# Kernel optimization log

Measured on AMD Instinct MI355X. Metric: run time of the kernel, lower is better.

Reference implementation:

```python
import jax, jax.numpy as jnp
import numpy as np

N_EMBD = 512
N_HEAD = 8
HEAD_DIM = N_EMBD // N_HEAD


def setup_inputs() -> dict:
    key = jax.random.key(0)
    ks = jax.random.split(key, 10)
    B, Tx, Tc, C = 8, 1024, 2048, N_EMBD
    s = 1.0 / np.sqrt(C)
    return {
        "x": jax.random.normal(ks[0], (B, Tx, C), dtype=jnp.float32),
        "context": jax.random.normal(ks[1], (B, Tc, C), dtype=jnp.float32),
        "Wq": jax.random.normal(ks[2], (C, C), dtype=jnp.float32) * s,
        "bq": jnp.zeros((C,), dtype=jnp.float32),
        "Wk": jax.random.normal(ks[3], (C, C), dtype=jnp.float32) * s,
        "bk": jnp.zeros((C,), dtype=jnp.float32),
        "Wv": jax.random.normal(ks[4], (C, C), dtype=jnp.float32) * s,
        "bv": jnp.zeros((C,), dtype=jnp.float32),
        "Wo": jax.random.normal(ks[5], (C, C), dtype=jnp.float32) * s,
        "bo": jnp.zeros((C,), dtype=jnp.float32),
    }


def reference(x, context, Wq, bq, Wk, bk, Wv, bv, Wo, bo):
    B, Tx, C = x.shape
    Tc = context.shape[1]
    nh, hd = N_HEAD, C // N_HEAD
    # projections (torch Linear: y = x @ W.T + b)
    q = (x @ Wq.T + bq).reshape(B, Tx, nh, hd).transpose(0, 2, 1, 3)
    k = (context @ Wk.T + bk).reshape(B, Tc, nh, hd).transpose(0, 2, 1, 3)
    v = (context @ Wv.T + bv).reshape(B, Tc, nh, hd).transpose(0, 2, 1, 3)
    # attention scores (B, nh, Tx, Tc)
    att = jnp.einsum("bhqd,bhkd->bhqk", q, k) * (1.0 / np.sqrt(hd))
    att = jax.nn.softmax(att, axis=-1)
    y = jnp.einsum("bhqk,bhkd->bhqd", att, v)
    y = y.transpose(0, 2, 1, 3).reshape(B, Tx, C)
    att_mean = att.mean(axis=1)  # (B, Tx, Tc)
    y = y @ Wo.T + bo
    return (y, att_mean)
```

## Files before the change

### kernel.cpp

```cpp
#include <hip/hip_runtime.h>

#define DEVI __device__ __forceinline__

typedef short bf16x8 __attribute__((ext_vector_type(8)));
typedef short bf16x4 __attribute__((ext_vector_type(4)));
typedef float f32x4 __attribute__((ext_vector_type(4)));

constexpr int Bb = 8, TX = 1024, TC = 2048, CC = 512, NH = 8, HD = 64;

DEVI unsigned short f2bf(float f) {
  union { float f; unsigned u; } v; v.f = f;
  return (unsigned short)((v.u + 0x7FFFu + ((v.u >> 16) & 1u)) >> 16);
}

DEVI unsigned cvtpk(float lo, float hi) {
  unsigned r;
  asm("v_cvt_pk_bf16_f32 %0, %1, %2" : "=v"(r) : "v"(lo), "v"(hi));
  return r;
}

DEVI f32x4 mfma16(bf16x8 a, bf16x8 b, f32x4 c) {
  return __builtin_amdgcn_mfma_f32_16x16x32_bf16(a, b, c, 0, 0, 0);
}

DEVI f32x4 zero4() { f32x4 z = {0.f, 0.f, 0.f, 0.f}; return z; }

__global__ __launch_bounds__(256) void cvt_bf16(
    const float* __restrict__ src, unsigned short* __restrict__ dst, int n8) {
  int i = blockIdx.x * 256 + threadIdx.x;
  const int stride = gridDim.x * 256;
  for (; i < n8; i += stride) {
    f32x4 a = *(const f32x4*)(src + (size_t)i * 8);
    f32x4 b = *(const f32x4*)(src + (size_t)i * 8 + 4);
    bf16x8 v;
#pragma unroll
    for (int j = 0; j < 4; j++) {
      v[j] = (short)f2bf(a[j]);
      v[j + 4] = (short)f2bf(b[j]);
    }
    *(bf16x8*)(dst + (size_t)i * 8) = v;
  }
}

template <int MODE>
__global__ __launch_bounds__(256) void proj_gemm(
    const unsigned short* __restrict__ A, const unsigned short* __restrict__ W,
    const float* __restrict__ bias, void* __restrict__ outp, int tlog2, float scale) {
  __shared__ __align__(16) unsigned short As[64 * 40];
  __shared__ __align__(16) unsigned short Bs[64 * 40];

  const int tid = threadIdx.x;
  const int wid = tid >> 6, l = tid & 63, l15 = l & 15, lhi = l >> 4;
  const int wm = wid >> 1, wn = wid & 1;
  const int mbase = blockIdx.y * 64, nbase = blockIdx.x * 64;
  const int sr = tid >> 2, sc0 = (tid & 3) * 8;

  f32x4 acc[2][2];
#pragma unroll
  for (int i = 0; i < 2; i++)
#pragma unroll
    for (int j = 0; j < 2; j++) acc[i][j] = zero4();

  for (int k0 = 0; k0 < CC; k0 += 32) {
    *(bf16x8*)&As[sr * 40 + sc0] =
        *(const bf16x8*)(A + (size_t)(mbase + sr) * CC + k0 + sc0);
    *(bf16x8*)&Bs[sr * 40 + sc0] =
        *(const bf16x8*)(W + (size_t)(nbase + sr) * CC + k0 + sc0);
    __syncthreads();

    bf16x8 a0 = *(const bf16x8*)&As[(wm * 32 + l15) * 40 + lhi * 8];
    bf16x8 a1 = *(const bf16x8*)&As[(wm * 32 + 16 + l15) * 40 + lhi * 8];
    bf16x8 b0 = *(const bf16x8*)&Bs[(wn * 32 + l15) * 40 + lhi * 8];
    bf16x8 b1 = *(const bf16x8*)&Bs[(wn * 32 + 16 + l15) * 40 + lhi * 8];
    acc[0][0] = mfma16(a0, b0, acc[0][0]);
    acc[0][1] = mfma16(a0, b1, acc[0][1]);
    acc[1][0] = mfma16(a1, b0, acc[1][0]);
    acc[1][1] = mfma16(a1, b1, acc[1][1]);
    __syncthreads();
  }

#pragma unroll
  for (int mi = 0; mi < 2; mi++)
#pragma unroll
    for (int ni = 0; ni < 2; ni++)
#pragma unroll
      for (int r = 0; r < 4; r++) {
        int grow = mbase + wm * 32 + mi * 16 + 4 * lhi + r;
        int gcol = nbase + wn * 32 + ni * 16 + l15;
        float val = (acc[mi][ni][r] + bias[gcol]) * scale;
        if (MODE == 0) {
          int T = 1 << tlog2;
          int bq = grow >> tlog2, tt = grow & (T - 1);
          int h = gcol >> 6, d = gcol & 63;
          size_t oidx = ((size_t)(bq * NH + h) * T + tt) * HD + d;
          ((unsigned short*)outp)[oidx] = f2bf(val);
        } else {
          ((float*)outp)[(size_t)grow * CC + gcol] = val;
        }
      }
}

__global__ __launch_bounds__(256) void kv_gemm(
    const unsigned short* __restrict__ A, const unsigned short* __restrict__ Wk,
    const unsigned short* __restrict__ Wv, const float* __restrict__ bk,
    const float* __restrict__ bv, unsigned short* __restrict__ k_out,
    unsigned short* __restrict__ v_out) {
  __shared__ __align__(16) unsigned short As[64 * 40];
  __shared__ __align__(16) unsigned short Bks[64 * 40];
  __shared__ __align__(16) unsigned short Bvs[64 * 40];

  const int tid = threadIdx.x;
  const int wid = tid >> 6, l = tid & 63, l15 = l & 15, lhi = l >> 4;
  const int wm = wid >> 1, wn = wid & 1;
  const int mbase = blockIdx.y * 64, nbase = blockIdx.x * 64;
  const int sr = tid >> 2, sc0 = (tid & 3) * 8;

  f32x4 acck[2][2], accv[2][2];
#pragma unroll
  for (int i = 0; i < 2; i++)
#pragma unroll
    for (int j = 0; j < 2; j++) { acck[i][j] = zero4(); accv[i][j] = zero4(); }

  for (int k0 = 0; k0 < CC; k0 += 32) {
    *(bf16x8*)&As[sr * 40 + sc0] =
        *(const bf16x8*)(A + (size_t)(mbase + sr) * CC + k0 + sc0);
    *(bf16x8*)&Bks[sr * 40 + sc0] =
        *(const bf16x8*)(Wk + (size_t)(nbase + sr) * CC + k0 + sc0);
    *(bf16x8*)&Bvs[sr * 40 + sc0] =
        *(const bf16x8*)(Wv + (size_t)(nbase + sr) * CC + k0 + sc0);
    __syncthreads();

    bf16x8 a0 = *(const bf16x8*)&As[(wm * 32 + l15) * 40 + lhi * 8];
    bf16x8 a1 = *(const bf16x8*)&As[(wm * 32 + 16 + l15) * 40 + lhi * 8];
    bf16x8 k0f = *(const bf16x8*)&Bks[(wn * 32 + l15) * 40 + lhi * 8];
    bf16x8 k1f = *(const bf16x8*)&Bks[(wn * 32 + 16 + l15) * 40 + lhi * 8];
    bf16x8 v0f = *(const bf16x8*)&Bvs[(wn * 32 + l15) * 40 + lhi * 8];
    bf16x8 v1f = *(const bf16x8*)&Bvs[(wn * 32 + 16 + l15) * 40 + lhi * 8];
    acck[0][0] = mfma16(a0, k0f, acck[0][0]);
    acck[0][1] = mfma16(a0, k1f, acck[0][1]);
    acck[1][0] = mfma16(a1, k0f, acck[1][0]);
    acck[1][1] = mfma16(a1, k1f, acck[1][1]);
    accv[0][0] = mfma16(a0, v0f, accv[0][0]);
    accv[0][1] = mfma16(a0, v1f, accv[0][1]);
    accv[1][0] = mfma16(a1, v0f, accv[1][0]);
    accv[1][1] = mfma16(a1, v1f, accv[1][1]);
    __syncthreads();
  }

#pragma unroll
  for (int mi = 0; mi < 2; mi++)
#pragma unroll
    for (int ni = 0; ni < 2; ni++)
#pragma unroll
      for (int r = 0; r < 4; r++) {
        int grow = mbase + wm * 32 + mi * 16 + 4 * lhi + r;
        int gcol = nbase + wn * 32 + ni * 16 + l15;
        int bq = grow >> 11, tt = grow & (TC - 1);
        int h = gcol >> 6, d = gcol & 63;
        float kv = acck[mi][ni][r] + bk[gcol];
        float vv = accv[mi][ni][r] + bv[gcol];
        k_out[((size_t)(bq * NH + h) * TC + tt) * HD + d] = f2bf(kv);
        v_out[((size_t)(bq * NH + h) * HD + d) * TC + tt] = f2bf(vv);
      }
}

__global__ __launch_bounds__(512) void attn_fwd(
    const unsigned short* __restrict__ Qw, const unsigned short* __restrict__ Kw,
    const unsigned short* __restrict__ Vtw, unsigned short* __restrict__ y_pre,
    float* __restrict__ m_ws, float* __restrict__ il_ws) {
  __shared__ __align__(16) unsigned short ktl[2][64 * 72];
  __shared__ __align__(16) unsigned short vtl[2][64 * 72];

  const int tid = threadIdx.x;
  const int wid = tid >> 6, l = tid & 63, l15 = l & 15, lhi = l >> 4;
  const int qg = blockIdx.x, h = blockIdx.y, b = blockIdx.z;
  const int qbase = qg * 128 + wid * 16;

  const unsigned short* Qh = Qw + (size_t)(b * NH + h) * TX * HD;
  const unsigned short* Kh = Kw + (size_t)(b * NH + h) * TC * HD;
  const unsigned short* Vt = Vtw + (size_t)(b * NH + h) * TC * HD;

  bf16x8 aq0 = *(const bf16x8*)(Qh + (size_t)(qbase + l15) * HD + lhi * 8);
  bf16x8 aq1 = *(const bf16x8*)(Qh + (size_t)(qbase + l15) * HD + 32 + lhi * 8);

  f32x4 accy[4];
#pragma unroll
  for (int db = 0; db < 4; db++) accy[db] = zero4();
  float mrun = -1e30f, lrun = 0.f;

  const int sl0 = l15 + ((lhi & 1) << 5);
  const int sl1 = sl0 + 16;
  const bool sel = ((lhi >> 1) & 1) != 0;

  const int sr = tid >> 3, sc0 = (tid & 7) * 8;

  bf16x8 kr = *(const bf16x8*)(Kh + (size_t)sr * HD + sc0);
  bf16x8 vp = *(const bf16x8*)(Vt + (size_t)sr * TC + sc0);
  *(bf16x8*)&ktl[0][sr * 72 + sc0] = kr;
  *(bf16x8*)&vtl[0][sr * 72 + sc0] = vp;
  __syncthreads();

  constexpr int NT = TC / 64;
  for (int kt = 0; kt < NT; kt++) {
    const int cur = kt & 1;

    if (kt + 1 < NT) {
      const int keyn = (kt + 1) * 64;
      kr = *(const bf16x8*)(Kh + (size_t)(keyn + sr) * HD + sc0);
      vp = *(const bf16x8*)(Vt + (size_t)sr * TC + keyn + sc0);
    }

    f32x4 s[4];
#pragma unroll
    for (int kb = 0; kb < 4; kb++) {
      bf16x8 bk0 = *(const bf16x8*)&ktl[cur][(kb * 16 + l15) * 72 + lhi * 8];
      bf16x8 bk1 = *(const bf16x8*)&ktl[cur][(kb * 16 + l15) * 72 + 32 + lhi * 8];
      f32x4 a = zero4();
      a = mfma16(bk0, aq0, a);
      a = mfma16(bk1, aq1, a);
      s[kb] = a;
    }

    float mx = s[0][0];
#pragma unroll
    for (int kb = 0; kb < 4; kb++)
#pragma unroll
      for (int r = 0; r < 4; r++) mx = fmaxf(mx, s[kb][r]);
    mx = fmaxf(mx, __shfl_xor(mx, 16));
    mx = fmaxf(mx, __shfl_xor(mx, 32));

    if (__any(mx - mrun > 5.0f)) {
      float mn = fmaxf(mrun, mx);
      float sc = __expf(mrun - mn);
      lrun *= sc;
      mrun = mn;
#pragma unroll
      for (int db = 0; db < 4; db++)
#pragma unroll
        for (int r = 0; r < 4; r++) accy[db][r] *= sc;
    }

    float p[4][4];
    float ps = 0.f;
#pragma unroll
    for (int kb = 0; kb < 4; kb++)
#pragma unroll
      for (int r = 0; r < 4; r++) {
        p[kb][r] = __expf(s[kb][r] - mrun);
        ps += p[kb][r];
      }
    ps += __shfl_xor(ps, 16);
    ps += __shfl_xor(ps, 32);
    lrun += ps;

    unsigned pkw[4][2];
#pragma unroll
    for (int kb = 0; kb < 4; kb++) {
      pkw[kb][0] = cvtpk(p[kb][0], p[kb][1]);
      pkw[kb][1] = cvtpk(p[kb][2], p[kb][3]);
    }
    unsigned a00 = (unsigned)__shfl((int)pkw[0][0], sl0);
    unsigned a01 = (unsigned)__shfl((int)pkw[0][1], sl0);
    unsigned a10 = (unsigned)__shfl((int)pkw[1][0], sl0);
    unsigned a11 = (unsigned)__shfl((int)pkw[1][1], sl0);
    unsigned c00 = (unsigned)__shfl((int)pkw[0][0], sl1);
    unsigned c01 = (unsigned)__shfl((int)pkw[0][1], sl1);
    unsigned c10 = (unsigned)__shfl((int)pkw[1][0], sl1);
    unsigned c11 = (unsigned)__shfl((int)pkw[1][1], sl1);
    unsigned e00 = (unsigned)__shfl((int)pkw[2][0], sl0);
    unsigned e01 = (unsigned)__shfl((int)pkw[2][1], sl0);
    unsigned e10 = (unsigned)__shfl((int)pkw[3][0], sl0);
    unsigned e11 = (unsigned)__shfl((int)pkw[3][1], sl0);
    unsigned g00 = (unsigned)__shfl((int)pkw[2][0], sl1);
    unsigned g01 = (unsigned)__shfl((int)pkw[2][1], sl1);
    unsigned g10 = (unsigned)__shfl((int)pkw[3][0], sl1);
    unsigned g11 = (unsigned)__shfl((int)pkw[3][1], sl1);
    union { unsigned u[4]; bf16x8 v; } B0, B1;
    B0.u[0] = sel ? a10 : a00;
    B0.u[1] = sel ? a11 : a01;
    B0.u[2] = sel ? c10 : c00;
    B0.u[3] = sel ? c11 : c01;
    B1.u[0] = sel ? e10 : e00;
    B1.u[1] = sel ? e11 : e01;
    B1.u[2] = sel ? g10 : g00;
    B1.u[3] = sel ? g11 : g01;

#pragma unroll
    for (int db = 0; db < 4; db++) {
      bf16x8 bv0 = *(const bf16x8*)&vtl[cur][(db * 16 + l15) * 72 + lhi * 8];
      bf16x8 bv1 = *(const bf16x8*)&vtl[cur][(db * 16 + l15) * 72 + 32 + lhi * 8];
      accy[db] = mfma16(bv0, B0.v, accy[db]);
      accy[db] = mfma16(bv1, B1.v, accy[db]);
    }

    if (kt + 1 < NT) {
      const int nxt = cur ^ 1;
      *(bf16x8*)&ktl[nxt][sr * 72 + sc0] = kr;
      *(bf16x8*)&vtl[nxt][sr * 72 + sc0] = vp;
    }
    __syncthreads();
  }

  const float il = 1.f / lrun;

#pragma unroll
  for (int db = 0; db < 4; db++) {
    bf16x4 o;
#pragma unroll
    for (int r = 0; r < 4; r++) o[r] = (short)f2bf(accy[db][r] * il);
    *(bf16x4*)(y_pre + (size_t)(b * TX + qbase + l15) * CC + h * HD + db * 16 +
               4 * lhi) = o;
  }
  if (lhi == 0) {
    int idx = (b * NH + h) * TX + qbase + l15;
    m_ws[idx] = mrun;
    il_ws[idx] = il;
  }
}

__global__ __launch_bounds__(256) void att_mean_k(
    const unsigned short* __restrict__ Qw, const unsigned short* __restrict__ Kw,
    const float* __restrict__ m_ws, const float* __restrict__ il_ws,
    float* __restrict__ attm) {
  __shared__ __align__(16) unsigned short ktl[2][64 * 72];

  const int tid = threadIdx.x;
  const int wid = tid >> 6, l = tid & 63, l15 = l & 15, lhi = l >> 4;
  const int qbase = blockIdx.x * 64 + wid * 16;
  const int keyb = blockIdx.y * 64;
  const int b = blockIdx.z;

  const unsigned short* Qb = Qw + (size_t)b * NH * TX * HD;
  const unsigned short* Kb = Kw + (size_t)b * NH * TC * HD;

  const int sr = tid >> 3, sc0 = (tid & 7) * 8;

  bf16x8 aq0[2], aq1[2];
  f32x4 mm[2], ii[2];

  auto load_q = [&](int h, int p) {
    const unsigned short* qp =
        Qb + ((size_t)h * TX + qbase + l15) * HD + lhi * 8;
    aq0[p] = *(const bf16x8*)qp;
    aq1[p] = *(const bf16x8*)(qp + 32);
    mm[p] = *(const f32x4*)(m_ws + (size_t)(b * NH + h) * TX + qbase + 4 * lhi);
    ii[p] = *(const f32x4*)(il_ws + (size_t)(b * NH + h) * TX + qbase + 4 * lhi);
  };

  bf16x8 kr0 = *(const bf16x8*)(Kb + ((size_t)keyb + sr) * HD + sc0);
  bf16x8 kr1 = *(const bf16x8*)(Kb + ((size_t)keyb + sr + 32) * HD + sc0);
  load_q(0, 0);
  *(bf16x8*)&ktl[0][sr * 72 + sc0] = kr0;
  *(bf16x8*)&ktl[0][(sr + 32) * 72 + sc0] = kr1;
  __syncthreads();

  f32x4 am[4];
#pragma unroll
  for (int kb = 0; kb < 4; kb++) am[kb] = zero4();

#pragma unroll
  for (int h = 0; h < NH; h++) {
    const int cur = h & 1;

    if (h + 1 < NH) {
      kr0 = *(const bf16x8*)(Kb + ((size_t)(h + 1) * TC + keyb + sr) * HD + sc0);
      kr1 = *(const bf16x8*)(Kb + ((size_t)(h + 1) * TC + keyb + sr + 32) * HD + sc0);
      load_q(h + 1, cur ^ 1);
    }

#pragma unroll
    for (int kb = 0; kb < 4; kb++) {
      bf16x8 bk0 = *(const bf16x8*)&ktl[cur][(kb * 16 + l15) * 72 + lhi * 8];
      bf16x8 bk1 = *(const bf16x8*)&ktl[cur][(kb * 16 + l15) * 72 + 32 + lhi * 8];
      f32x4 a = zero4();
      a = mfma16(aq0[cur], bk0, a);
      a = mfma16(aq1[cur], bk1, a);
#pragma unroll
      for (int r = 0; r < 4; r++)
        am[kb][r] += __expf(a[r] - mm[cur][r]) * ii[cur][r];
    }

    if (h + 1 < NH) {
      const int nxt = cur ^ 1;
      *(bf16x8*)&ktl[nxt][sr * 72 + sc0] = kr0;
      *(bf16x8*)&ktl[nxt][(sr + 32) * 72 + sc0] = kr1;
    }
    __syncthreads();
  }

#pragma unroll
  for (int kb = 0; kb < 4; kb++)
#pragma unroll
    for (int r = 0; r < 4; r++) {
      int trow = qbase + 4 * lhi + r;
      attm[(size_t)(b * TX + trow) * TC + keyb + kb * 16 + l15] = am[kb][r] * 0.125f;
    }
}

extern "C" void kernel_launch(void* const* d_in, const int* in_sizes, int n_in,
                              void* d_out, int out_size, void* d_ws, size_t ws_size,
                              hipStream_t stream) {
  const float* x   = (const float*)d_in[0];
  const float* ctx = (const float*)d_in[1];
  const float* Wq  = (const float*)d_in[2];
  const float* bq  = (const float*)d_in[3];
  const float* Wk  = (const float*)d_in[4];
  const float* bk  = (const float*)d_in[5];
  const float* Wv  = (const float*)d_in[6];
  const float* bv  = (const float*)d_in[7];
  const float* Wo  = (const float*)d_in[8];
  const float* bo  = (const float*)d_in[9];

  float* y_out = (float*)d_out;
  float* attm  = y_out + (size_t)Bb * TX * CC;

  unsigned short* q_ws = (unsigned short*)d_ws;
  unsigned short* k_ws = q_ws + (size_t)Bb * NH * TX * HD;
  unsigned short* v_ws = k_ws + (size_t)Bb * NH * TC * HD;
  float* m_ws  = (float*)(v_ws + (size_t)Bb * NH * TC * HD);
  float* il_ws = m_ws + (size_t)Bb * NH * TX;
  unsigned short* y_pre = (unsigned short*)(il_ws + (size_t)Bb * NH * TX);
  unsigned short* wb = y_pre + (size_t)Bb * TX * CC;
  unsigned short* wbq = wb, *wbk = wb + CC * CC, *wbv = wb + 2 * CC * CC,
                 *wbo = wb + 3 * CC * CC;

  unsigned short* xb = k_ws;
  unsigned short* cb = (unsigned short*)attm;

  const int NX8 = Bb * TX * CC / 8, NC8 = Bb * TC * CC / 8, NW8 = CC * CC / 8;
  cvt_bf16<<<dim3(2048), 256, 0, stream>>>(x, xb, NX8);
  cvt_bf16<<<dim3(2048), 256, 0, stream>>>(ctx, cb, NC8);
  cvt_bf16<<<dim3(128), 256, 0, stream>>>(Wq, wbq, NW8);
  cvt_bf16<<<dim3(128), 256, 0, stream>>>(Wk, wbk, NW8);
  cvt_bf16<<<dim3(128), 256, 0, stream>>>(Wv, wbv, NW8);
  cvt_bf16<<<dim3(128), 256, 0, stream>>>(Wo, wbo, NW8);

  proj_gemm<0><<<dim3(CC / 64, (Bb * TX) / 64), 256, 0, stream>>>(xb, wbq, bq, q_ws, 10, 0.125f);
  kv_gemm<<<dim3(CC / 64, (Bb * TC) / 64), 256, 0, stream>>>(cb, wbk, wbv, bk, bv, k_ws, v_ws);
  attn_fwd<<<dim3(TX / 128, NH, Bb), 512, 0, stream>>>(q_ws, k_ws, v_ws, y_pre, m_ws, il_ws);
  att_mean_k<<<dim3(TX / 64, TC / 64, Bb), 256, 0, stream>>>(q_ws, k_ws, m_ws, il_ws, attm);
  proj_gemm<1><<<dim3(CC / 64, (Bb * TX) / 64), 256, 0, stream>>>(y_pre, wbo, bo, y_out, 10, 1.0f);
}
```

Baseline: 225.0 us.

## Swizzle K/V shared-memory tiles and fold log2e into Q scale for exp2

Replaces the padded 72-element LDS row stride with an unpadded 64-element layout using an XOR swizzle on 16-byte chunks for both the stores and the MFMA operand reads. Folds log2(e) into the Q projection scale so both attention kernels can use exp2 instead of exp. Raises the lazy-rescale threshold to match the log2 domain. The swizzle is meant to avoid bank conflicts without padding, and exp2 drops a multiply per exponential.

```diff
diff --git a/kernel.cpp b/kernel.cpp
--- a/kernel.cpp
+++ b/kernel.cpp
@@ -7,6 +7,7 @@
 typedef float f32x4 __attribute__((ext_vector_type(4)));
 
 constexpr int Bb = 8, TX = 1024, TC = 2048, CC = 512, NH = 8, HD = 64;
+constexpr float LOG2E = 1.44269504f;
 
 DEVI unsigned short f2bf(float f) {
   union { float f; unsigned u; } v; v.f = f;
@@ -168,8 +169,8 @@
     const unsigned short* __restrict__ Qw, const unsigned short* __restrict__ Kw,
     const unsigned short* __restrict__ Vtw, unsigned short* __restrict__ y_pre,
     float* __restrict__ m_ws, float* __restrict__ il_ws) {
-  __shared__ __align__(16) unsigned short ktl[2][64 * 72];
-  __shared__ __align__(16) unsigned short vtl[2][64 * 72];
+  __shared__ __align__(16) unsigned short ktl[2][64 * 64];
+  __shared__ __align__(16) unsigned short vtl[2][64 * 64];
 
   const int tid = threadIdx.x;
   const int wid = tid >> 6, l = tid & 63, l15 = l & 15, lhi = l >> 4;
@@ -192,12 +193,17 @@
   const int sl1 = sl0 + 16;
   const bool sel = ((lhi >> 1) & 1) != 0;
 
-  const int sr = tid >> 3, sc0 = (tid & 7) * 8;
+  const int rs0 = (lhi ^ (l15 & 7)) << 3;
+  const int rs1 = ((lhi ^ 4) ^ (l15 & 7)) << 3;
+
+  const int sr = tid >> 3;
+  const int ssw = ((tid & 7) ^ (sr & 7)) << 3;
+  const int sc0 = (tid & 7) * 8;
 
   bf16x8 kr = *(const bf16x8*)(Kh + (size_t)sr * HD + sc0);
   bf16x8 vp = *(const bf16x8*)(Vt + (size_t)sr * TC + sc0);
-  *(bf16x8*)&ktl[0][sr * 72 + sc0] = kr;
-  *(bf16x8*)&vtl[0][sr * 72 + sc0] = vp;
+  *(bf16x8*)&ktl[0][sr * 64 + ssw] = kr;
+  *(bf16x8*)&vtl[0][sr * 64 + ssw] = vp;
   __syncthreads();
 
   constexpr int NT = TC / 64;
@@ -213,8 +219,8 @@
     f32x4 s[4];
 #pragma unroll
     for (int kb = 0; kb < 4; kb++) {
-      bf16x8 bk0 = *(const bf16x8*)&ktl[cur][(kb * 16 + l15) * 72 + lhi * 8];
-      bf16x8 bk1 = *(const bf16x8*)&ktl[cur][(kb * 16 + l15) * 72 + 32 + lhi * 8];
+      bf16x8 bk0 = *(const bf16x8*)&ktl[cur][(kb * 16 + l15) * 64 + rs0];
+      bf16x8 bk1 = *(const bf16x8*)&ktl[cur][(kb * 16 + l15) * 64 + rs1];
       f32x4 a = zero4();
       a = mfma16(bk0, aq0, a);
       a = mfma16(bk1, aq1, a);
@@ -229,9 +235,9 @@
     mx = fmaxf(mx, __shfl_xor(mx, 16));
     mx = fmaxf(mx, __shfl_xor(mx, 32));
 
-    if (__any(mx - mrun > 5.0f)) {
+    if (__any(mx - mrun > 7.0f)) {
       float mn = fmaxf(mrun, mx);
-      float sc = __expf(mrun - mn);
+      float sc = exp2f(mrun - mn);
       lrun *= sc;
       mrun = mn;
 #pragma unroll
@@ -246,7 +252,7 @@
     for (int kb = 0; kb < 4; kb++)
 #pragma unroll
       for (int r = 0; r < 4; r++) {
-        p[kb][r] = __expf(s[kb][r] - mrun);
+        p[kb][r] = exp2f(s[kb][r] - mrun);
         ps += p[kb][r];
       }
     ps += __shfl_xor(ps, 16);
@@ -287,16 +293,16 @@
 
 #pragma unroll
     for (int db = 0; db < 4; db++) {
-      bf16x8 bv0 = *(const bf16x8*)&vtl[cur][(db * 16 + l15) * 72 + lhi * 8];
-      bf16x8 bv1 = *(const bf16x8*)&vtl[cur][(db * 16 + l15) * 72 + 32 + lhi * 8];
+      bf16x8 bv0 = *(const bf16x8*)&vtl[cur][(db * 16 + l15) * 64 + rs0];
+      bf16x8 bv1 = *(const bf16x8*)&vtl[cur][(db * 16 + l15) * 64 + rs1];
       accy[db] = mfma16(bv0, B0.v, accy[db]);
       accy[db] = mfma16(bv1, B1.v, accy[db]);
     }
 
     if (kt + 1 < NT) {
       const int nxt = cur ^ 1;
-      *(bf16x8*)&ktl[nxt][sr * 72 + sc0] = kr;
-      *(bf16x8*)&vtl[nxt][sr * 72 + sc0] = vp;
+      *(bf16x8*)&ktl[nxt][sr * 64 + ssw] = kr;
+      *(bf16x8*)&vtl[nxt][sr * 64 + ssw] = vp;
     }
     __syncthreads();
   }
@@ -322,7 +328,7 @@
     const unsigned short* __restrict__ Qw, const unsigned short* __restrict__ Kw,
     const float* __restrict__ m_ws, const float* __restrict__ il_ws,
     float* __restrict__ attm) {
-  __shared__ __align__(16) unsigned short ktl[2][64 * 72];
+  __shared__ __align__(16) unsigned short ktl[2][64 * 64];
 
   const int tid = threadIdx.x;
   const int wid = tid >> 6, l = tid & 63, l15 = l & 15, lhi = l >> 4;
@@ -333,7 +339,12 @@
   const unsigned short* Qb = Qw + (size_t)b * NH * TX * HD;
   const unsigned short* Kb = Kw + (size_t)b * NH * TC * HD;
 
-  const int sr = tid >> 3, sc0 = (tid & 7) * 8;
+  const int rs0 = (lhi ^ (l15 & 7)) << 3;
+  const int rs1 = ((lhi ^ 4) ^ (l15 & 7)) << 3;
+
+  const int sr = tid >> 3;
+  const int ssw = ((tid & 7) ^ (sr & 7)) << 3;
+  const int sc0 = (tid & 7) * 8;
 
   bf16x8 aq0[2], aq1[2];
   f32x4 mm[2], ii[2];
@@ -350,8 +361,8 @@
   bf16x8 kr0 = *(const bf16x8*)(Kb + ((size_t)keyb + sr) * HD + sc0);
   bf16x8 kr1 = *(const bf16x8*)(Kb + ((size_t)keyb + sr + 32) * HD + sc0);
   load_q(0, 0);
-  *(bf16x8*)&ktl[0][sr * 72 + sc0] = kr0;
-  *(bf16x8*)&ktl[0][(sr + 32) * 72 + sc0] = kr1;
+  *(bf16x8*)&ktl[0][sr * 64 + ssw] = kr0;
+  *(bf16x8*)&ktl[0][(sr + 32) * 64 + ssw] = kr1;
   __syncthreads();
 
   f32x4 am[4];
@@ -370,20 +381,20 @@
 
 #pragma unroll
     for (int kb = 0; kb < 4; kb++) {
-      bf16x8 bk0 = *(const bf16x8*)&ktl[cur][(kb * 16 + l15) * 72 + lhi * 8];
-      bf16x8 bk1 = *(const bf16x8*)&ktl[cur][(kb * 16 + l15) * 72 + 32 + lhi * 8];
+      bf16x8 bk0 = *(const bf16x8*)&ktl[cur][(kb * 16 + l15) * 64 + rs0];
+      bf16x8 bk1 = *(const bf16x8*)&ktl[cur][(kb * 16 + l15) * 64 + rs1];
       f32x4 a = zero4();
       a = mfma16(aq0[cur], bk0, a);
       a = mfma16(aq1[cur], bk1, a);
 #pragma unroll
       for (int r = 0; r < 4; r++)
-        am[kb][r] += __expf(a[r] - mm[cur][r]) * ii[cur][r];
+        am[kb][r] += exp2f(a[r] - mm[cur][r]) * ii[cur][r];
     }
 
     if (h + 1 < NH) {
       const int nxt = cur ^ 1;
-      *(bf16x8*)&ktl[nxt][sr * 72 + sc0] = kr0;
-      *(bf16x8*)&ktl[nxt][(sr + 32) * 72 + sc0] = kr1;
+      *(bf16x8*)&ktl[nxt][sr * 64 + ssw] = kr0;
+      *(bf16x8*)&ktl[nxt][(sr + 32) * 64 + ssw] = kr1;
     }
     __syncthreads();
   }
@@ -435,7 +446,8 @@
   cvt_bf16<<<dim3(128), 256, 0, stream>>>(Wv, wbv, NW8);
   cvt_bf16<<<dim3(128), 256, 0, stream>>>(Wo, wbo, NW8);
 
-  proj_gemm<0><<<dim3(CC / 64, (Bb * TX) / 64), 256, 0, stream>>>(xb, wbq, bq, q_ws, 10, 0.125f);
+  proj_gemm<0><<<dim3(CC / 64, (Bb * TX) / 64), 256, 0, stream>>>(
+      xb, wbq, bq, q_ws, 10, 0.125f * LOG2E);
   kv_gemm<<<dim3(CC / 64, (Bb * TC) / 64), 256, 0, stream>>>(cb, wbk, wbv, bk, bv, k_ws, v_ws);
   attn_fwd<<<dim3(TX / 128, NH, Bb), 512, 0, stream>>>(q_ws, k_ws, v_ws, y_pre, m_ws, il_ws);
   att_mean_k<<<dim3(TX / 64, TC / 64, Bb), 256, 0, stream>>>(q_ws, k_ws, m_ws, il_ws, attm);
```

New measurement: 252.2 us. 12.1% more time.
